# Optimization experiments

Hardware: AMD Instinct MI355X
Metric: run time of the kernel (lower is better)

## Reference

```python
import jax, jax.numpy as jnp
import numpy as np


def _graph_conv(x, W, b, src, dst, norm_src, norm_dst, n_nodes):
    # DGL GraphConv, norm='both': out = D_in^{-1/2} * A * D_out^{-1/2} * x * W + b
    h = x * norm_src[:, None]                      # [N, d] scale by src out-degree norm
    m = h[src]                                     # [E, d] gather (irregular access)
    agg = jax.ops.segment_sum(m, dst, num_segments=n_nodes)  # [N, d] scatter-add
    agg = agg * norm_dst[:, None]
    return agg @ W + b


def setup_inputs() -> dict:
    key = jax.random.key(0)
    ks = jax.random.split(key, 6)
    N, E, IN, HID = 50000, 800000, 64, 128
    in_feat = jax.random.normal(ks[0], (N, IN), dtype=jnp.float32)
    W1 = jax.random.normal(ks[1], (IN, HID), dtype=jnp.float32) * (1.0 / np.sqrt(IN))
    b1 = jnp.zeros((HID,), dtype=jnp.float32)
    W2 = jax.random.normal(ks[2], (HID, IN), dtype=jnp.float32) * (1.0 / np.sqrt(HID))
    b2 = jnp.zeros((IN,), dtype=jnp.float32)
    src = jax.random.randint(ks[3], (E,), 0, N, dtype=jnp.int32)
    dst = jax.random.randint(ks[4], (E,), 0, N, dtype=jnp.int32)
    return {"in_feat": in_feat, "W1": W1, "b1": b1, "W2": W2, "b2": b2,
            "src": src, "dst": dst, "n_nodes": N}


def reference(in_feat, W1, b1, W2, b2, src, dst, n_nodes):
    ones = jnp.ones(src.shape, dtype=in_feat.dtype)
    deg_out = jax.ops.segment_sum(ones, src, num_segments=n_nodes)
    deg_in = jax.ops.segment_sum(ones, dst, num_segments=n_nodes)
    # DGL clamps degrees to min 1 (allow_zero_in_degree=True just skips the check)
    norm_src = jnp.clip(deg_out, 1.0, None) ** -0.5
    norm_dst = jnp.clip(deg_in, 1.0, None) ** -0.5
    h = _graph_conv(in_feat, W1, b1, src, dst, norm_src, norm_dst, n_nodes)
    h = jax.nn.relu(h)
    h = _graph_conv(h, W2, b2, src, dst, norm_src, norm_dst, n_nodes)
    return h
```

## Files before the change

### kernel.cpp

```cpp
#include <hip/hip_runtime.h>

#define IN_F 64
#define HID_F 128
#define CAP 64
#define CHUNK 4096
#define CAPB 4096
#define MAXB 512

typedef unsigned short u16;
typedef unsigned int u32;
typedef _Float16 f16;
typedef __attribute__((ext_vector_type(4))) _Float16 f16x4;
typedef __attribute__((ext_vector_type(8))) _Float16 f16x8;
typedef __attribute__((ext_vector_type(4))) float f32x4;

__global__ __launch_bounds__(256)
void partition_kernel(const int* __restrict__ src, const int* __restrict__ dst,
                      int* __restrict__ gcurD, int* __restrict__ gcurS,
                      u32* __restrict__ bufD, u16* __restrict__ bufS,
                      const float* __restrict__ W1, const float* __restrict__ W2,
                      f16* __restrict__ W1t, f16* __restrict__ W2t,
                      int E, int NBUCK) {
    if (blockIdx.x == gridDim.x - 1) {
        for (int t = threadIdx.x; t < 2 * IN_F * HID_F; t += 256) {
            if (t < IN_F * HID_F) {
                int n = t / IN_F, k = t % IN_F;
                W1t[t] = (f16)W1[k * HID_F + n];
            } else {
                int i = t - IN_F * HID_F;
                int n = i / HID_F, k = i % HID_F;
                W2t[i] = (f16)W2[k * IN_F + n];
            }
        }
        return;
    }
    __shared__ int histD[MAXB], histS[MAXB], baseD[MAXB], baseS[MAXB];
    const int t  = threadIdx.x;
    const int e0 = blockIdx.x * CHUNK;
    const int n  = min(CHUNK, E - e0);

    for (int b = t; b < NBUCK; b += 256) { histD[b] = 0; histS[b] = 0; }
    __syncthreads();
    for (int i = t; i < n; i += 256) {
        atomicAdd(&histD[dst[e0 + i] >> 7], 1);
        atomicAdd(&histS[src[e0 + i] >> 7], 1);
    }
    __syncthreads();
    for (int b = t; b < NBUCK; b += 256) {
        baseD[b] = atomicAdd(&gcurD[b], histD[b]);
        baseS[b] = atomicAdd(&gcurS[b], histS[b]);
        histD[b] = 0;
        histS[b] = 0;
    }
    __syncthreads();
    for (int i = t; i < n; i += 256) {
        int d  = dst[e0 + i];
        int s  = src[e0 + i];
        int bD = d >> 7, bS = s >> 7;
        int p  = baseD[bD] + atomicAdd(&histD[bD], 1);
        if (p < CAPB) bufD[(size_t)bD * CAPB + p] = (u32)d | ((u32)s << 16);
        int p2 = baseS[bS] + atomicAdd(&histS[bS], 1);
        if (p2 < CAPB) bufS[(size_t)bS * CAPB + p2] = (u16)s;
    }
}

__global__ __launch_bounds__(256)
void bucket_pass2_kernel(const u32* __restrict__ bufD, const int* __restrict__ gcurD,
                         const u16* __restrict__ bufS, const int* __restrict__ gcurS,
                         u16* __restrict__ slots, int* __restrict__ deg_in,
                         float* __restrict__ norm_dst, float* __restrict__ norm_src,
                         const float* __restrict__ x, f16x4* __restrict__ scaled_x,
                         int N, int NBUCK) {
    __shared__ int lcur[128];
    const int t = threadIdx.x;
    if (t < 128) lcur[t] = 0;
    __syncthreads();
    if (blockIdx.x < NBUCK) {
        const int b = blockIdx.x;
        const int cnt = min(gcurD[b], CAPB);
        const u32* p = bufD + (size_t)b * CAPB;
        for (int i = t; i < cnt; i += 256) {
            u32 v = p[i];
            int d = (int)(v & 0xFFFFu);
            int s = (int)(v >> 16);
            int pos = atomicAdd(&lcur[d & 127], 1);
            if (pos < CAP) slots[(size_t)d * CAP + pos] = (u16)s;
        }
        __syncthreads();
        int node = b * 128 + t;
        if (t < 128 && node < N) {
            deg_in[node]   = lcur[t];
            norm_dst[node] = rsqrtf((float)max(lcur[t], 1));
        }
    } else {
        const int b = blockIdx.x - NBUCK;
        const int cnt = min(gcurS[b], CAPB);
        const u16* p = bufS + (size_t)b * CAPB;
        for (int i = t; i < cnt; i += 256)
            atomicAdd(&lcur[p[i] & 127], 1);
        __syncthreads();
        int node0 = b * 128;
        if (t < 128 && node0 + t < N)
            norm_src[node0 + t] = rsqrtf((float)max(lcur[t], 1));
        for (int i = t; i < 128 * 16; i += 256) {
            int r = i >> 4, c = i & 15;
            int node = node0 + r;
            if (node < N) {
                float ns = rsqrtf((float)max(lcur[r], 1));
                float4 v = ((const float4*)x)[(size_t)node * 16 + c];
                f16x4 h;
                h.x = (f16)(v.x * ns); h.y = (f16)(v.y * ns);
                h.z = (f16)(v.z * ns); h.w = (f16)(v.w * ns);
                scaled_x[(size_t)node * 16 + c] = h;
            }
        }
    }
}

__global__ __launch_bounds__(256)
void gather_gemm_kernel(const f16x4* __restrict__ x, const u16* __restrict__ slots,
                        const int* __restrict__ deg_in,
                        const f16* __restrict__ W1t, const float* __restrict__ b1,
                        const float* __restrict__ nd, const float* __restrict__ ns,
                        const f16* __restrict__ W2t, f16* __restrict__ g2, int N) {
    constexpr int LDX = IN_F + 8;
    constexpr int LDH = HID_F + 8;
    __shared__ f16 sx[64 * LDX];
    __shared__ f16 h[4][16 * LDH];

    const int t   = threadIdx.x;
    const int row = t >> 4;
    const int c   = t & 15;

#pragma unroll
    for (int rr = row; rr < 64; rr += 16) {
        const int node = blockIdx.x * 64 + rr;
        float4 acc = make_float4(0.f, 0.f, 0.f, 0.f);
        if (node < N) {
            int deg = min(deg_in[node], CAP);
            const u16* srow = slots + (size_t)node * CAP;
            int i = 0;
            for (; i + 8 <= deg; i += 8) {
                int s[8];
#pragma unroll
                for (int j = 0; j < 8; ++j) s[j] = (int)srow[i + j];
                f16x4 v[8];
#pragma unroll
                for (int j = 0; j < 8; ++j) v[j] = x[(size_t)s[j] * 16 + c];
#pragma unroll
                for (int j = 0; j < 8; ++j) {
                    acc.x += (float)v[j].x; acc.y += (float)v[j].y;
                    acc.z += (float)v[j].z; acc.w += (float)v[j].w;
                }
            }
            for (; i < deg; ++i) {
                f16x4 v = x[(size_t)srow[i] * 16 + c];
                acc.x += (float)v.x; acc.y += (float)v.y;
                acc.z += (float)v.z; acc.w += (float)v.w;
            }
        }
        f16x4 hv;
        hv.x = (f16)acc.x; hv.y = (f16)acc.y; hv.z = (f16)acc.z; hv.w = (f16)acc.w;
        *(f16x4*)&sx[rr * LDX + c * 4] = hv;
    }
    __syncthreads();

    const int wave = t >> 6;
    const int lane = t & 63;
    const int nl   = lane & 15;
    const int quad = lane >> 4;
    const int r0   = blockIdx.x * 64 + wave * 16;
    f16* hw = h[wave];

    f16x8 a1[2];
#pragma unroll
    for (int kf = 0; kf < 2; ++kf)
        a1[kf] = *(const f16x8*)(sx + (wave * 16 + nl) * LDX + kf * 32 + quad * 8);

    f32x4 acc1[8];
#pragma unroll
    for (int ct = 0; ct < 8; ++ct) {
        acc1[ct] = (f32x4){0.f, 0.f, 0.f, 0.f};
#pragma unroll
        for (int kf = 0; kf < 2; ++kf) {
            f16x8 b = *(const f16x8*)(W1t + (ct * 16 + nl) * IN_F + kf * 32 + quad * 8);
            acc1[ct] = __builtin_amdgcn_mfma_f32_16x16x32_f16(a1[kf], b, acc1[ct], 0, 0, 0);
        }
    }

    float rs1[4];
#pragma unroll
    for (int reg = 0; reg < 4; ++reg)
        rs1[reg] = nd[min(r0 + quad * 4 + reg, N - 1)];
#pragma unroll
    for (int ct = 0; ct < 8; ++ct) {
        float bb = b1[ct * 16 + nl];
#pragma unroll
        for (int reg = 0; reg < 4; ++reg) {
            float v = fmaxf(acc1[ct][reg] * rs1[reg] + bb, 0.f);
            hw[(quad * 4 + reg) * LDH + ct * 16 + nl] = (f16)v;
        }
    }
    __builtin_amdgcn_s_waitcnt(0);

    f16x8 a2[4];
#pragma unroll
    for (int kf = 0; kf < 4; ++kf)
        a2[kf] = *(const f16x8*)(hw + nl * LDH + kf * 32 + quad * 8);

    f32x4 acc2[4];
#pragma unroll
    for (int ct = 0; ct < 4; ++ct) {
        acc2[ct] = (f32x4){0.f, 0.f, 0.f, 0.f};
#pragma unroll
        for (int kf = 0; kf < 4; ++kf) {
            f16x8 b = *(const f16x8*)(W2t + (ct * 16 + nl) * HID_F + kf * 32 + quad * 8);
            acc2[ct] = __builtin_amdgcn_mfma_f32_16x16x32_f16(a2[kf], b, acc2[ct], 0, 0, 0);
        }
    }

    float rs2[4];
#pragma unroll
    for (int reg = 0; reg < 4; ++reg)
        rs2[reg] = ns[min(r0 + quad * 4 + reg, N - 1)];
#pragma unroll
    for (int ct = 0; ct < 4; ++ct)
#pragma unroll
        for (int reg = 0; reg < 4; ++reg) {
            int r = r0 + quad * 4 + reg;
            if (r < N)
                g2[(size_t)r * IN_F + ct * 16 + nl] = (f16)(acc2[ct][reg] * rs2[reg]);
        }
}

__global__ void gather_out_kernel(const f16x4* __restrict__ x, const u16* __restrict__ slots,
                                  const int* __restrict__ deg_in, const float* __restrict__ sd,
                                  const float* __restrict__ bias,
                                  float4* __restrict__ out, int N) {
    int t = blockIdx.x * blockDim.x + threadIdx.x;
    int node = t >> 4;
    int c = t & 15;
    if (node >= N) return;
    int deg = min(deg_in[node], CAP);
    const u16* srow = slots + (size_t)node * CAP;
    float4 acc = make_float4(0.f, 0.f, 0.f, 0.f);

    int i = 0;
    for (; i + 8 <= deg; i += 8) {
        int s[8];
#pragma unroll
        for (int j = 0; j < 8; ++j) s[j] = (int)srow[i + j];
        f16x4 v[8];
#pragma unroll
        for (int j = 0; j < 8; ++j) v[j] = x[(size_t)s[j] * 16 + c];
#pragma unroll
        for (int j = 0; j < 8; ++j) {
            acc.x += (float)v[j].x; acc.y += (float)v[j].y;
            acc.z += (float)v[j].z; acc.w += (float)v[j].w;
        }
    }
    for (; i < deg; ++i) {
        f16x4 v = x[(size_t)srow[i] * 16 + c];
        acc.x += (float)v.x; acc.y += (float)v.y;
        acc.z += (float)v.z; acc.w += (float)v.w;
    }
    float d = sd[node];
    float4 bb = ((const float4*)bias)[c];
    acc.x = acc.x * d + bb.x;
    acc.y = acc.y * d + bb.y;
    acc.z = acc.z * d + bb.z;
    acc.w = acc.w * d + bb.w;
    out[t] = acc;
}

extern "C" void kernel_launch(void* const* d_in, const int* in_sizes, int n_in,
                              void* d_out, int out_size, void* d_ws, size_t ws_size,
                              hipStream_t stream) {
    const float* in_feat = (const float*)d_in[0];
    const float* W1      = (const float*)d_in[1];
    const float* b1      = (const float*)d_in[2];
    const float* W2      = (const float*)d_in[3];
    const float* b2      = (const float*)d_in[4];
    const int*   src     = (const int*)d_in[5];
    const int*   dst     = (const int*)d_in[6];

    const int N = in_sizes[0] / IN_F;
    const int E = in_sizes[5];
    float* out = (float*)d_out;

    const int NBUCK = (N + 127) >> 7;

    int* deg_in  = (int*)d_ws;
    int* gcurD   = deg_in + N;
    int* gcurS   = gcurD + MAXB;
    u16* slots   = (u16*)(gcurS + MAXB);
    float* norm_src = (float*)(slots + (size_t)N * CAP);
    float* norm_dst = norm_src + N;
    f16* scaled_x = (f16*)(norm_dst + N);
    f16* g2       = scaled_x + (size_t)N * IN_F;
    f16* W1t      = g2 + (size_t)N * IN_F;
    f16* W2t      = W1t + IN_F * HID_F;
    u32* bufD     = (u32*)(W2t + IN_F * HID_F);
    u16* bufS     = (u16*)(bufD + (size_t)NBUCK * CAPB);

    hipMemsetAsync(gcurD, 0, sizeof(int) * 2 * MAXB, stream);
    partition_kernel<<<(E + CHUNK - 1) / CHUNK + 1, 256, 0, stream>>>(
        src, dst, gcurD, gcurS, bufD, bufS, W1, W2, W1t, W2t, E, NBUCK);

    bucket_pass2_kernel<<<2 * NBUCK, 256, 0, stream>>>(
        bufD, gcurD, bufS, gcurS, slots, deg_in, norm_dst, norm_src,
        in_feat, (f16x4*)scaled_x, N, NBUCK);

    gather_gemm_kernel<<<(N + 63) / 64, 256, 0, stream>>>(
        (const f16x4*)scaled_x, slots, deg_in, W1t, b1, norm_dst, norm_src,
        W2t, g2, N);

    gather_out_kernel<<<(N * 16 + 255) / 256, 256, 0, stream>>>(
        (const f16x4*)g2, slots, deg_in, norm_dst, b2, (float4*)out, N);
}
```

Before: 184.5 us.

## Shrink gather-GEMM tiles to 16 nodes per block and split columns across waves

The fused gather+two-layer GEMM kernel now handles 16 nodes per block instead of 64. Each thread gathers one node, and the four waves divide the output column tiles of both matmuls rather than each wave owning its own 16 rows. This gives four times as many blocks and cuts per-thread serial gather work and register use, which should help latency hiding on the irregular gather. In exchange, each block reloads W1t/W2t for fewer rows and needs an extra block-wide barrier between the two matmuls.

```diff
diff --git a/kernel.cpp b/kernel.cpp
--- a/kernel.cpp
+++ b/kernel.cpp
@@ -125,43 +125,43 @@
                         const f16* __restrict__ W2t, f16* __restrict__ g2, int N) {
     constexpr int LDX = IN_F + 8;
     constexpr int LDH = HID_F + 8;
-    __shared__ f16 sx[64 * LDX];
-    __shared__ f16 h[4][16 * LDH];
+    __shared__ __align__(16) f16 sx[16 * LDX];
+    __shared__ __align__(16) f16 h[16 * LDH];
 
     const int t   = threadIdx.x;
     const int row = t >> 4;
     const int c   = t & 15;
-
-#pragma unroll
-    for (int rr = row; rr < 64; rr += 16) {
-        const int node = blockIdx.x * 64 + rr;
-        float4 acc = make_float4(0.f, 0.f, 0.f, 0.f);
-        if (node < N) {
-            int deg = min(deg_in[node], CAP);
-            const u16* srow = slots + (size_t)node * CAP;
-            int i = 0;
-            for (; i + 8 <= deg; i += 8) {
-                int s[8];
-#pragma unroll
-                for (int j = 0; j < 8; ++j) s[j] = (int)srow[i + j];
-                f16x4 v[8];
-#pragma unroll
-                for (int j = 0; j < 8; ++j) v[j] = x[(size_t)s[j] * 16 + c];
-#pragma unroll
-                for (int j = 0; j < 8; ++j) {
-                    acc.x += (float)v[j].x; acc.y += (float)v[j].y;
-                    acc.z += (float)v[j].z; acc.w += (float)v[j].w;
-                }
+    const int r0  = blockIdx.x * 16;
+    const int node = r0 + row;
+
+    float4 acc = make_float4(0.f, 0.f, 0.f, 0.f);
+    if (node < N) {
+        int deg = min(deg_in[node], CAP);
+        const u16* srow = slots + (size_t)node * CAP;
+        int i = 0;
+        for (; i + 8 <= deg; i += 8) {
+            int s[8];
+#pragma unroll
+            for (int j = 0; j < 8; ++j) s[j] = (int)srow[i + j];
+            f16x4 v[8];
+#pragma unroll
+            for (int j = 0; j < 8; ++j) v[j] = x[(size_t)s[j] * 16 + c];
+#pragma unroll
+            for (int j = 0; j < 8; ++j) {
+                acc.x += (float)v[j].x; acc.y += (float)v[j].y;
+                acc.z += (float)v[j].z; acc.w += (float)v[j].w;
             }
-            for (; i < deg; ++i) {
-                f16x4 v = x[(size_t)srow[i] * 16 + c];
-                acc.x += (float)v.x; acc.y += (float)v.y;
-                acc.z += (float)v.z; acc.w += (float)v.w;
-            }
-        }
+        }
+        for (; i < deg; ++i) {
+            f16x4 v = x[(size_t)srow[i] * 16 + c];
+            acc.x += (float)v.x; acc.y += (float)v.y;
+            acc.z += (float)v.z; acc.w += (float)v.w;
+        }
+    }
+    {
         f16x4 hv;
         hv.x = (f16)acc.x; hv.y = (f16)acc.y; hv.z = (f16)acc.z; hv.w = (f16)acc.w;
-        *(f16x4*)&sx[rr * LDX + c * 4] = hv;
+        *(f16x4*)&sx[row * LDX + c * 4] = hv;
     }
     __syncthreads();
 
@@ -169,54 +169,41 @@
     const int lane = t & 63;
     const int nl   = lane & 15;
     const int quad = lane >> 4;
-    const int r0   = blockIdx.x * 64 + wave * 16;
-    f16* hw = h[wave];
 
     f16x8 a1[2];
 #pragma unroll
     for (int kf = 0; kf < 2; ++kf)
-        a1[kf] = *(const f16x8*)(sx + (wave * 16 + nl) * LDX + kf * 32 + quad * 8);
-
-    f32x4 acc1[8];
-#pragma unroll
-    for (int ct = 0; ct < 8; ++ct) {
-        acc1[ct] = (f32x4){0.f, 0.f, 0.f, 0.f};
+        a1[kf] = *(const f16x8*)(sx + nl * LDX + kf * 32 + quad * 8);
+
+    float rs1[4];
+#pragma unroll
+    for (int reg = 0; reg < 4; ++reg)
+        rs1[reg] = nd[min(r0 + quad * 4 + reg, N - 1)];
+
+#pragma unroll
+    for (int cti = 0; cti < 2; ++cti) {
+        const int ct = wave * 2 + cti;
+        f32x4 acc1 = (f32x4){0.f, 0.f, 0.f, 0.f};
 #pragma unroll
         for (int kf = 0; kf < 2; ++kf) {
             f16x8 b = *(const f16x8*)(W1t + (ct * 16 + nl) * IN_F + kf * 32 + quad * 8);
-            acc1[ct] = __builtin_amdgcn_mfma_f32_16x16x32_f16(a1[kf], b, acc1[ct], 0, 0, 0);
-        }
-    }
-
-    float rs1[4];
-#pragma unroll
-    for (int reg = 0; reg < 4; ++reg)
-        rs1[reg] = nd[min(r0 + quad * 4 + reg, N - 1)];
-#pragma unroll
-    for (int ct = 0; ct < 8; ++ct) {
+            acc1 = __builtin_amdgcn_mfma_f32_16x16x32_f16(a1[kf], b, acc1, 0, 0, 0);
+        }
         float bb = b1[ct * 16 + nl];
 #pragma unroll
         for (int reg = 0; reg < 4; ++reg) {
-            float v = fmaxf(acc1[ct][reg] * rs1[reg] + bb, 0.f);
-            hw[(quad * 4 + reg) * LDH + ct * 16 + nl] = (f16)v;
-        }
-    }
-    __builtin_amdgcn_s_waitcnt(0);
-
-    f16x8 a2[4];
-#pragma unroll
-    for (int kf = 0; kf < 4; ++kf)
-        a2[kf] = *(const f16x8*)(hw + nl * LDH + kf * 32 + quad * 8);
-
-    f32x4 acc2[4];
-#pragma unroll
-    for (int ct = 0; ct < 4; ++ct) {
-        acc2[ct] = (f32x4){0.f, 0.f, 0.f, 0.f};
-#pragma unroll
-        for (int kf = 0; kf < 4; ++kf) {
-            f16x8 b = *(const f16x8*)(W2t + (ct * 16 + nl) * HID_F + kf * 32 + quad * 8);
-            acc2[ct] = __builtin_amdgcn_mfma_f32_16x16x32_f16(a2[kf], b, acc2[ct], 0, 0, 0);
-        }
+            float v = fmaxf(acc1[reg] * rs1[reg] + bb, 0.f);
+            h[(quad * 4 + reg) * LDH + ct * 16 + nl] = (f16)v;
+        }
+    }
+    __syncthreads();
+
+    f32x4 acc2 = (f32x4){0.f, 0.f, 0.f, 0.f};
+#pragma unroll
+    for (int kf = 0; kf < 4; ++kf) {
+        f16x8 a2 = *(const f16x8*)(h + nl * LDH + kf * 32 + quad * 8);
+        f16x8 b  = *(const f16x8*)(W2t + (wave * 16 + nl) * HID_F + kf * 32 + quad * 8);
+        acc2 = __builtin_amdgcn_mfma_f32_16x16x32_f16(a2, b, acc2, 0, 0, 0);
     }
 
     float rs2[4];
@@ -224,13 +211,11 @@
     for (int reg = 0; reg < 4; ++reg)
         rs2[reg] = ns[min(r0 + quad * 4 + reg, N - 1)];
 #pragma unroll
-    for (int ct = 0; ct < 4; ++ct)
-#pragma unroll
-        for (int reg = 0; reg < 4; ++reg) {
-            int r = r0 + quad * 4 + reg;
-            if (r < N)
-                g2[(size_t)r * IN_F + ct * 16 + nl] = (f16)(acc2[ct][reg] * rs2[reg]);
-        }
+    for (int reg = 0; reg < 4; ++reg) {
+        int r = r0 + quad * 4 + reg;
+        if (r < N)
+            g2[(size_t)r * IN_F + wave * 16 + nl] = (f16)(acc2[reg] * rs2[reg]);
+    }
 }
 
 __global__ void gather_out_kernel(const f16x4* __restrict__ x, const u16* __restrict__ slots,
@@ -311,7 +296,7 @@
         bufD, gcurD, bufS, gcurS, slots, deg_in, norm_dst, norm_src,
         in_feat, (f16x4*)scaled_x, N, NBUCK);
 
-    gather_gemm_kernel<<<(N + 63) / 64, 256, 0, stream>>>(
+    gather_gemm_kernel<<<(N + 15) / 16, 256, 0, stream>>>(
         (const f16x4*)scaled_x, slots, deg_in, W1t, b1, norm_dst, norm_src,
         W2t, g2, N);
 
```

Result: faster. 169.2 us (-8.3%).
